# Optimization experiments

Hardware: AMD Instinct MI355X
Metric: run time of the kernel (lower is better)

Reference implementation:

```python
import jax, jax.numpy as jnp
import numpy as np

CONTEXT = 3  # config['context']
B, H, W = 8, 256, 256
NBR = 2 * CONTEXT  # number of similarity branches


def _conv(x, w, b):
    # x: [N, Cin, H, W], w: [Cout, Cin, kh, kw], SAME padding, stride 1
    y = jax.lax.conv_general_dilated(x, w, (1, 1), 'SAME',
                                     dimension_numbers=('NCHW', 'OIHW', 'NCHW'))
    return y + b[None, :, None, None]


def setup_inputs() -> dict:
    key = jax.random.key(0)
    ks = jax.random.split(key, 5)
    x = jax.random.normal(ks[0], (B, 2 * CONTEXT + 1, H, W), dtype=jnp.float32)
    # kaiming-ish scaled inits
    W1 = jax.random.normal(ks[1], (NBR, 64, 2, 3, 3), dtype=jnp.float32) * (2.0 / (64 * 9)) ** 0.5
    b1 = jnp.zeros((NBR, 64), dtype=jnp.float32)
    W2 = jax.random.normal(ks[2], (NBR, 1, 64, 1, 1), dtype=jnp.float32) * (2.0 / 1) ** 0.5 * 0.1
    b2 = jnp.zeros((NBR, 1), dtype=jnp.float32)
    Wm = jax.random.normal(ks[3], (7, 7, 3, 3), dtype=jnp.float32) * (2.0 / (7 * 9)) ** 0.5
    bm = jnp.zeros((7,), dtype=jnp.float32)
    return {'x': x, 'W1': W1, 'b1': b1, 'W2': W2, 'b2': b2, 'Wm': Wm, 'bm': bm}


def reference(x, W1, b1, W2, b2, Wm, bm):
    # mode == 'context' path just returns x; this implements the main path.
    base = x[:, CONTEXT:CONTEXT + 1]                                  # [B,1,H,W]
    checks = jnp.concatenate([x[:, :CONTEXT], x[:, CONTEXT + 1:]], axis=1)  # [B,6,H,W]
    check_e = checks[:, :, None]                                      # [B,6,1,H,W]
    base_e = jnp.broadcast_to(base[:, None], check_e.shape)           # [B,6,1,H,W]
    # channel order: pre-frames -> (base, check); post-frames -> (check, base)
    ch0 = jnp.concatenate([base_e[:, :CONTEXT], check_e[:, CONTEXT:]], axis=2 - 2 + 2)  # placeholder
    ch0 = jnp.concatenate([base_e[:, :CONTEXT], check_e[:, CONTEXT:]], axis=1)
    ch1 = jnp.concatenate([check_e[:, :CONTEXT], base_e[:, CONTEXT:]], axis=1)
    pairs = jnp.concatenate([ch0, ch1], axis=2)                       # [B,6,2,H,W]
    pairs = jnp.swapaxes(pairs, 0, 1)                                 # [6,B,2,H,W]

    def branch(pair, w1, bb1, w2, bb2):
        h = jax.nn.relu(_conv(pair, w1, bb1))                         # [B,64,H,W]
        return jax.nn.sigmoid(_conv(h, w2, bb2))                      # [B,1,H,W]

    sims = jax.vmap(branch)(pairs, W1, b1, W2, b2)                    # [6,B,1,H,W]
    weighted = sims[:, :, 0] * jnp.swapaxes(checks, 0, 1)             # [6,B,H,W]
    weighted = jnp.swapaxes(weighted, 0, 1)                           # [B,6,H,W]
    combined = jnp.concatenate([weighted[:, :CONTEXT], base, weighted[:, CONTEXT:]], axis=1)  # [B,7,H,W]
    return _conv(combined, Wm, bm)                                    # [B,7,H,W]
```

## Files before the change

### kernel.cpp

```cpp
#include <hip/hip_runtime.h>
#include <math.h>

#define Bn 8
#define Hn 256
#define Wn 256
#define HW (Hn * Wn)
#define ROWS 8
#define RP 264

typedef __attribute__((ext_vector_type(8))) short bf16x8;
typedef __attribute__((ext_vector_type(4))) float f32x4;

__device__ __forceinline__ unsigned int pk_bits(unsigned int lo,
                                                unsigned int hi) {
  return __builtin_amdgcn_perm(hi, lo, 0x07060302u);
}
__device__ __forceinline__ unsigned int pk_bf16(float lo, float hi) {
  return pk_bits(__float_as_uint(lo), __float_as_uint(hi));
}

__global__ __launch_bounds__(256) void sim_kernel(
    const float* __restrict__ x,
    const float* __restrict__ W1,
    const float* __restrict__ b1,
    const float* __restrict__ W2,
    const float* __restrict__ b2,
    float* __restrict__ comb)
{
  __shared__ float rowsF[2 * 10 * RP];
  __shared__ uint4 wq[4][64];

  int bi = blockIdx.x;
  int n  = bi >> 8;
  int b  = (bi >> 5) & 7;
  int h0 = (bi & 31) * ROWS;
  int cc = (n < 3) ? n : n + 1;
  int t = threadIdx.x;

  const float* xb     = x + (size_t)b * 7 * HW;
  const float* basep  = xb + 3 * HW;
  const float* checkp = xb + (size_t)cc * HW;

  {
    int f = t >> 6, qq = (t >> 4) & 3, m = t & 15;
    int ch = 16 * f + m;
    int bsrc = (n < 3) ? 0 : 1;
    const float* wch = W1 + ((size_t)(n * 64 + ch)) * 18;
    unsigned int kv[4];
#pragma unroll
    for (int jj = 0; jj < 4; ++jj) {
      int k0 = qq * 8 + jj * 2, k1 = k0 + 1;
      float v0 = 0.f, v1 = 0.f;
      if (k0 < 18) {
        int src = (k0 < 9) ? bsrc : 1 - bsrc;
        v0 = wch[src * 9 + (k0 < 9 ? k0 : k0 - 9)];
      }
      if (k1 < 18) {
        int src = (k1 < 9) ? bsrc : 1 - bsrc;
        v1 = wch[src * 9 + (k1 < 9 ? k1 : k1 - 9)];
      }
      kv[jj] = pk_bf16(v0, v1);
    }
    wq[f][(qq << 4) + m] = make_uint4(kv[0], kv[1], kv[2], kv[3]);
  }

  int lane = t & 63, wvid = t >> 6;
  int q = lane >> 4, m_ = lane & 15;
  float w2v[4][4], b1v[4][4];
#pragma unroll
  for (int f = 0; f < 4; ++f) {
    float4 tw = *(const float4*)&W2[n * 64 + 16 * f + 4 * q];
    float4 tb = *(const float4*)&b1[n * 64 + 16 * f + 4 * q];
    w2v[f][0] = tw.x; w2v[f][1] = tw.y; w2v[f][2] = tw.z; w2v[f][3] = tw.w;
    b1v[f][0] = tb.x; b1v[f][1] = tb.y; b1v[f][2] = tb.z; b1v[f][3] = tb.w;
  }
  float bb = b2[n];

  {
    int col = (t & 63) << 2;
#pragma unroll
    for (int it = 0; it < 5; ++it) {
      int rf = it * 4 + (t >> 6);
      int pl = (rf >= 10) ? 1 : 0;
      int j  = rf - pl * 10;
      int hh = h0 - 1 + j;
      const float* src = pl ? checkp : basep;
      float4 val = make_float4(0.f, 0.f, 0.f, 0.f);
      if ((unsigned)hh < (unsigned)Hn)
        val = *(const float4*)(src + hh * Wn + col);
      *(float4*)&rowsF[rf * RP + 4 + col] = val;
    }
    if (t < 20) {
      rowsF[t * RP + 3] = 0.f;
      rowsF[t * RP + 260] = 0.f;
    }
    if (t == 20) rowsF[0] = 0.f;
  }

  const unsigned int* rowsU = (const unsigned int*)rowsF;
  unsigned int addr[8], vbit[8];
#pragma unroll
  for (int jh = 0; jh < 8; ++jh) {
    int k = 8 * q + jh;
    if (k < 18) {
      int pl = (k >= 9) ? 1 : 0;
      int rem = k - 9 * pl;
      int rr = rem / 3, dx = rem - rr * 3;
      addr[jh] = (pl * 10 + rr) * RP + 3 + dx + wvid * 64 + m_;
      vbit[jh] = 1u;
    } else {
      addr[jh] = 0u;
      vbit[jh] = 0u;
    }
  }

  __syncthreads();

  bf16x8 afrag[4];
#pragma unroll
  for (int f = 0; f < 4; ++f) afrag[f] = *(const bf16x8*)&wq[f][lane];

  float* combcc = comb + ((size_t)b * 7 + cc) * HW;
  float* comb3  = comb + ((size_t)b * 7 + 3) * HW;
  int pxs = wvid * 64 + lane;

#pragma unroll 1
  for (int r = 0; r < ROWS; ++r) {
    int h = h0 + r;

    float g[4];
#pragma unroll
    for (int i = 0; i < 4; ++i) {
      unsigned int offs = (unsigned)(r * RP + i * 16);

      unsigned int d[8];
#pragma unroll
      for (int jh = 0; jh < 8; ++jh)
        d[jh] = rowsU[addr[jh] + vbit[jh] * offs];

      union { unsigned int u[4]; bf16x8 v; } bu;
#pragma unroll
      for (int jj = 0; jj < 4; ++jj)
        bu.u[jj] = pk_bits(d[2 * jj], d[2 * jj + 1]);
      bf16x8 bfrag = bu.v;

      f32x4 acc[4];
#pragma unroll
      for (int f = 0; f < 4; ++f) {
        acc[f][0] = b1v[f][0]; acc[f][1] = b1v[f][1];
        acc[f][2] = b1v[f][2]; acc[f][3] = b1v[f][3];
      }
#pragma unroll
      for (int f = 0; f < 4; ++f)
        acc[f] = __builtin_amdgcn_mfma_f32_16x16x32_bf16(afrag[f], bfrag,
                                                         acc[f], 0, 0, 0);

      float sp = 0.f;
#pragma unroll
      for (int f = 0; f < 4; ++f)
#pragma unroll
        for (int rr = 0; rr < 4; ++rr)
          sp = fmaf(w2v[f][rr], fmaxf(acc[f][rr], 0.f), sp);
      sp += __shfl_xor(sp, 16, 64);
      sp += __shfl_xor(sp, 32, 64);
      sp += bb;

      float e = __builtin_amdgcn_exp2f(sp * -1.442695041f);
      g[i] = __builtin_amdgcn_rcpf(1.f + e);
    }

    int hi = lane >> 4;
    float gsel = (hi == 0) ? g[0] : (hi == 1) ? g[1] : (hi == 2) ? g[2] : g[3];
    float ccv = rowsF[(10 + r + 1) * RP + 4 + pxs];
    combcc[h * Wn + pxs] = gsel * ccv;
    if (n == 0) comb3[h * Wn + pxs] = rowsF[(r + 1) * RP + 4 + pxs];
  }
}

__global__ __launch_bounds__(256) void mix_kernel(
    const float* __restrict__ comb,
    const float* __restrict__ Wm,
    const float* __restrict__ bm,
    float* __restrict__ out)
{
  __shared__ float mr[7 * 6 * RP];

  int bi = blockIdx.x;
  int b  = bi >> 6;
  int h0 = (bi & 63) << 2;
  int t = threadIdx.x;

  for (int u = t; u < 42 * 64; u += 256) {
    int rf = u >> 6;
    int col = (u & 63) << 2;
    int ic = rf / 6, j = rf - ic * 6;
    int hh = h0 - 1 + j;
    float4 v = make_float4(0.f, 0.f, 0.f, 0.f);
    if ((unsigned)hh < (unsigned)Hn)
      v = *(const float4*)(comb + ((size_t)b * 7 + ic) * HW + hh * Wn + col);
    *(float4*)&mr[rf * RP + 4 + col] = v;
  }
  if (t < 42) {
    mr[t * RP + 3] = 0.f;
    mr[t * RP + 260] = 0.f;
  }
  __syncthreads();

  int r   = t >> 6;
  int px0 = (t & 63) << 2;
  int h   = h0 + r;

  float acc[7][4];
#pragma unroll
  for (int oc = 0; oc < 7; ++oc) {
    float bv = bm[oc];
#pragma unroll
    for (int p = 0; p < 4; ++p) acc[oc][p] = bv;
  }

#pragma unroll 1
  for (int ic = 0; ic < 7; ++ic) {
    float w[3][12];
#pragma unroll
    for (int dy = 0; dy < 3; ++dy) {
      const float* rp = &mr[(ic * 6 + r + dy) * RP];
      *(float4*)&w[dy][0] = *(const float4*)(rp + px0);
      *(float4*)&w[dy][4] = *(const float4*)(rp + px0 + 4);
      *(float4*)&w[dy][8] = *(const float4*)(rp + px0 + 8);
    }
    const float* wp = Wm + ic * 9;
#pragma unroll
    for (int oc = 0; oc < 7; ++oc) {
      const float* wo = wp + oc * 63;
#pragma unroll
      for (int dy = 0; dy < 3; ++dy)
#pragma unroll
        for (int dx = 0; dx < 3; ++dx) {
          float wvv = wo[dy * 3 + dx];
#pragma unroll
          for (int p = 0; p < 4; ++p)
            acc[oc][p] = fmaf(wvv, w[dy][3 + p + dx], acc[oc][p]);
        }
    }
  }

  float* ob = out + (size_t)b * 7 * HW + h * Wn + px0;
#pragma unroll
  for (int oc = 0; oc < 7; ++oc)
    *(float4*)(ob + (size_t)oc * HW) =
        make_float4(acc[oc][0], acc[oc][1], acc[oc][2], acc[oc][3]);
}

extern "C" void kernel_launch(void* const* d_in, const int* in_sizes, int n_in,
                              void* d_out, int out_size, void* d_ws, size_t ws_size,
                              hipStream_t stream) {
  const float* x  = (const float*)d_in[0];
  const float* W1 = (const float*)d_in[1];
  const float* b1 = (const float*)d_in[2];
  const float* W2 = (const float*)d_in[3];
  const float* b2 = (const float*)d_in[4];
  const float* Wm = (const float*)d_in[5];
  const float* bm = (const float*)d_in[6];
  float* out  = (float*)d_out;
  float* comb = (float*)d_ws;

  sim_kernel<<<6 * 8 * (Hn / ROWS), 256, 0, stream>>>(x, W1, b1, W2, b2, comb);
  mix_kernel<<<8 * (Hn / 4), 256, 0, stream>>>(comb, Wm, bm, out);
}
```

Measured before the change: 121.6 us.

## Reorder MFMA K taps, batch LDS loads, pass bias as accumulator, shrink mix tiles

In the similarity kernel the 18 conv taps are permuted across the K lanes through constant lookup tables. Padding lanes now read a dedicated zero strip instead of address 0. LDS reads for two 16-pixel groups are issued together per half, and the b1 vector is passed directly as the MFMA accumulator input, which cuts register copies. The mix kernel switches from 4 rows by 4 pixels to 2 rows by 2 pixels per thread and doubles the block count, trading extra halo reloads (4 rows loaded per 2 output rows) for more parallelism and fewer registers per thread.

```diff
diff --git a/kernel.cpp b/kernel.cpp
--- a/kernel.cpp
+++ b/kernel.cpp
@@ -7,6 +7,7 @@
 #define HW (Hn * Wn)
 #define ROWS 8
 #define RP 264
+#define ZW (20 * RP)
 
 typedef __attribute__((ext_vector_type(8))) short bf16x8;
 typedef __attribute__((ext_vector_type(4))) float f32x4;
@@ -18,6 +19,10 @@
 __device__ __forceinline__ unsigned int pk_bf16(float lo, float hi) {
   return pk_bits(__float_as_uint(lo), __float_as_uint(hi));
 }
+
+__device__ __constant__ const int T0c[8] = {0, 1, 2, 9, 10, 11, 3, 4};
+__device__ __constant__ const int T1c[8] = {6, 7, 8, 15, 16, 17, 12, 13};
+__device__ __constant__ const int T2c[8] = {5, 14, -1, -1, -1, -1, -1, -1};
 
 __global__ __launch_bounds__(256) void sim_kernel(
     const float* __restrict__ x,
@@ -27,7 +32,7 @@
     const float* __restrict__ b2,
     float* __restrict__ comb)
 {
-  __shared__ float rowsF[2 * 10 * RP];
+  __shared__ float rowsF[20 * RP + 64];
   __shared__ uint4 wq[4][64];
 
   int bi = blockIdx.x;
@@ -43,36 +48,41 @@
 
   {
     int f = t >> 6, qq = (t >> 4) & 3, m = t & 15;
-    int ch = 16 * f + m;
     int bsrc = (n < 3) ? 0 : 1;
-    const float* wch = W1 + ((size_t)(n * 64 + ch)) * 18;
+    const float* wch = W1 + ((size_t)(n * 64 + 16 * f + m)) * 18;
     unsigned int kv[4];
 #pragma unroll
     for (int jj = 0; jj < 4; ++jj) {
-      int k0 = qq * 8 + jj * 2, k1 = k0 + 1;
-      float v0 = 0.f, v1 = 0.f;
-      if (k0 < 18) {
-        int src = (k0 < 9) ? bsrc : 1 - bsrc;
-        v0 = wch[src * 9 + (k0 < 9 ? k0 : k0 - 9)];
-      }
-      if (k1 < 18) {
-        int src = (k1 < 9) ? bsrc : 1 - bsrc;
-        v1 = wch[src * 9 + (k1 < 9 ? k1 : k1 - 9)];
-      }
-      kv[jj] = pk_bf16(v0, v1);
+      int ja = 2 * jj, jb = 2 * jj + 1;
+      int ta = (qq == 0) ? T0c[ja] : (qq == 1) ? T1c[ja]
+               : (qq == 2) ? T2c[ja] : -1;
+      int tb = (qq == 0) ? T0c[jb] : (qq == 1) ? T1c[jb]
+               : (qq == 2) ? T2c[jb] : -1;
+      float va = 0.f, vb = 0.f;
+      if (ta >= 0) {
+        int pl = ta / 9, rem = ta - pl * 9;
+        va = wch[(pl ? 1 - bsrc : bsrc) * 9 + rem];
+      }
+      if (tb >= 0) {
+        int pl = tb / 9, rem = tb - pl * 9;
+        vb = wch[(pl ? 1 - bsrc : bsrc) * 9 + rem];
+      }
+      kv[jj] = pk_bf16(va, vb);
     }
     wq[f][(qq << 4) + m] = make_uint4(kv[0], kv[1], kv[2], kv[3]);
   }
 
   int lane = t & 63, wvid = t >> 6;
   int q = lane >> 4, m_ = lane & 15;
-  float w2v[4][4], b1v[4][4];
+  float w2v[4][4];
+  f32x4 b1vv[4];
 #pragma unroll
   for (int f = 0; f < 4; ++f) {
     float4 tw = *(const float4*)&W2[n * 64 + 16 * f + 4 * q];
     float4 tb = *(const float4*)&b1[n * 64 + 16 * f + 4 * q];
     w2v[f][0] = tw.x; w2v[f][1] = tw.y; w2v[f][2] = tw.z; w2v[f][3] = tw.w;
-    b1v[f][0] = tb.x; b1v[f][1] = tb.y; b1v[f][2] = tb.z; b1v[f][3] = tb.w;
+    b1vv[f][0] = tb.x; b1vv[f][1] = tb.y;
+    b1vv[f][2] = tb.z; b1vv[f][3] = tb.w;
   }
   float bb = b2[n];
 
@@ -94,22 +104,22 @@
       rowsF[t * RP + 3] = 0.f;
       rowsF[t * RP + 260] = 0.f;
     }
-    if (t == 20) rowsF[0] = 0.f;
+    if (t >= 192) rowsF[ZW + (t - 192)] = 0.f;
   }
 
   const unsigned int* rowsU = (const unsigned int*)rowsF;
   unsigned int addr[8], vbit[8];
 #pragma unroll
   for (int jh = 0; jh < 8; ++jh) {
-    int k = 8 * q + jh;
-    if (k < 18) {
-      int pl = (k >= 9) ? 1 : 0;
-      int rem = k - 9 * pl;
+    int tap = (q == 0) ? T0c[jh] : (q == 1) ? T1c[jh]
+              : (q == 2) ? T2c[jh] : -1;
+    if (tap >= 0) {
+      int pl = tap / 9, rem = tap - pl * 9;
       int rr = rem / 3, dx = rem - rr * 3;
       addr[jh] = (pl * 10 + rr) * RP + 3 + dx + wvid * 64 + m_;
       vbit[jh] = 1u;
     } else {
-      addr[jh] = 0u;
+      addr[jh] = (unsigned)ZW;
       vbit[jh] = 0u;
     }
   }
@@ -127,46 +137,48 @@
 #pragma unroll 1
   for (int r = 0; r < ROWS; ++r) {
     int h = h0 + r;
+    unsigned int rowoff = (unsigned)(r * RP);
+
+    unsigned int base[8];
+#pragma unroll
+    for (int jh = 0; jh < 8; ++jh) base[jh] = addr[jh] + vbit[jh] * rowoff;
 
     float g[4];
 #pragma unroll
-    for (int i = 0; i < 4; ++i) {
-      unsigned int offs = (unsigned)(r * RP + i * 16);
-
-      unsigned int d[8];
-#pragma unroll
-      for (int jh = 0; jh < 8; ++jh)
-        d[jh] = rowsU[addr[jh] + vbit[jh] * offs];
-
-      union { unsigned int u[4]; bf16x8 v; } bu;
-#pragma unroll
-      for (int jj = 0; jj < 4; ++jj)
-        bu.u[jj] = pk_bits(d[2 * jj], d[2 * jj + 1]);
-      bf16x8 bfrag = bu.v;
-
-      f32x4 acc[4];
-#pragma unroll
-      for (int f = 0; f < 4; ++f) {
-        acc[f][0] = b1v[f][0]; acc[f][1] = b1v[f][1];
-        acc[f][2] = b1v[f][2]; acc[f][3] = b1v[f][3];
-      }
-#pragma unroll
-      for (int f = 0; f < 4; ++f)
-        acc[f] = __builtin_amdgcn_mfma_f32_16x16x32_bf16(afrag[f], bfrag,
-                                                         acc[f], 0, 0, 0);
-
-      float sp = 0.f;
-#pragma unroll
-      for (int f = 0; f < 4; ++f)
-#pragma unroll
-        for (int rr = 0; rr < 4; ++rr)
-          sp = fmaf(w2v[f][rr], fmaxf(acc[f][rr], 0.f), sp);
-      sp += __shfl_xor(sp, 16, 64);
-      sp += __shfl_xor(sp, 32, 64);
-      sp += bb;
-
-      float e = __builtin_amdgcn_exp2f(sp * -1.442695041f);
-      g[i] = __builtin_amdgcn_rcpf(1.f + e);
+    for (int half = 0; half < 2; ++half) {
+      unsigned int dlo[8], dhi[8];
+#pragma unroll
+      for (int jh = 0; jh < 8; ++jh) {
+        dlo[jh] = rowsU[base[jh] + half * 32];
+        dhi[jh] = rowsU[base[jh] + half * 32 + 16];
+      }
+#pragma unroll
+      for (int j = 0; j < 2; ++j) {
+        const unsigned int* d = j ? dhi : dlo;
+        union { unsigned int u[4]; bf16x8 v; } bu;
+#pragma unroll
+        for (int jj = 0; jj < 4; ++jj)
+          bu.u[jj] = pk_bits(d[2 * jj], d[2 * jj + 1]);
+
+        f32x4 acc[4];
+#pragma unroll
+        for (int f = 0; f < 4; ++f)
+          acc[f] = __builtin_amdgcn_mfma_f32_16x16x32_bf16(afrag[f], bu.v,
+                                                           b1vv[f], 0, 0, 0);
+
+        float sp = 0.f;
+#pragma unroll
+        for (int f = 0; f < 4; ++f)
+#pragma unroll
+          for (int rr = 0; rr < 4; ++rr)
+            sp = fmaf(w2v[f][rr], fmaxf(acc[f][rr], 0.f), sp);
+        sp += __shfl_xor(sp, 16, 64);
+        sp += __shfl_xor(sp, 32, 64);
+        sp += bb;
+
+        float e = __builtin_amdgcn_exp2f(sp * -1.442695041f);
+        g[2 * half + j] = __builtin_amdgcn_rcpf(1.f + e);
+      }
     }
 
     int hi = lane >> 4;
@@ -183,50 +195,49 @@
     const float* __restrict__ bm,
     float* __restrict__ out)
 {
-  __shared__ float mr[7 * 6 * RP];
+  __shared__ float mr[28 * RP];
 
   int bi = blockIdx.x;
-  int b  = bi >> 6;
-  int h0 = (bi & 63) << 2;
+  int b  = bi >> 7;
+  int h0 = (bi & 127) << 1;
   int t = threadIdx.x;
 
-  for (int u = t; u < 42 * 64; u += 256) {
+  for (int u = t; u < 28 * 64; u += 256) {
     int rf = u >> 6;
     int col = (u & 63) << 2;
-    int ic = rf / 6, j = rf - ic * 6;
+    int ic = rf >> 2, j = rf & 3;
     int hh = h0 - 1 + j;
     float4 v = make_float4(0.f, 0.f, 0.f, 0.f);
     if ((unsigned)hh < (unsigned)Hn)
       v = *(const float4*)(comb + ((size_t)b * 7 + ic) * HW + hh * Wn + col);
     *(float4*)&mr[rf * RP + 4 + col] = v;
   }
-  if (t < 42) {
+  if (t < 28) {
     mr[t * RP + 3] = 0.f;
     mr[t * RP + 260] = 0.f;
   }
   __syncthreads();
 
-  int r   = t >> 6;
-  int px0 = (t & 63) << 2;
+  int r   = t >> 7;
+  int px0 = (t & 127) << 1;
   int h   = h0 + r;
 
-  float acc[7][4];
+  float acc[7][2];
 #pragma unroll
   for (int oc = 0; oc < 7; ++oc) {
     float bv = bm[oc];
-#pragma unroll
-    for (int p = 0; p < 4; ++p) acc[oc][p] = bv;
+    acc[oc][0] = bv;
+    acc[oc][1] = bv;
   }
 
 #pragma unroll 1
   for (int ic = 0; ic < 7; ++ic) {
-    float w[3][12];
+    float w[3][4];
 #pragma unroll
     for (int dy = 0; dy < 3; ++dy) {
-      const float* rp = &mr[(ic * 6 + r + dy) * RP];
-      *(float4*)&w[dy][0] = *(const float4*)(rp + px0);
-      *(float4*)&w[dy][4] = *(const float4*)(rp + px0 + 4);
-      *(float4*)&w[dy][8] = *(const float4*)(rp + px0 + 8);
+      const float* rp = &mr[(ic * 4 + r + dy) * RP + 3 + px0];
+      w[dy][0] = rp[0]; w[dy][1] = rp[1];
+      w[dy][2] = rp[2]; w[dy][3] = rp[3];
     }
     const float* wp = Wm + ic * 9;
 #pragma unroll
@@ -237,9 +248,8 @@
 #pragma unroll
         for (int dx = 0; dx < 3; ++dx) {
           float wvv = wo[dy * 3 + dx];
-#pragma unroll
-          for (int p = 0; p < 4; ++p)
-            acc[oc][p] = fmaf(wvv, w[dy][3 + p + dx], acc[oc][p]);
+          acc[oc][0] = fmaf(wvv, w[dy][0 + dx], acc[oc][0]);
+          acc[oc][1] = fmaf(wvv, w[dy][1 + dx], acc[oc][1]);
         }
     }
   }
@@ -247,8 +257,7 @@
   float* ob = out + (size_t)b * 7 * HW + h * Wn + px0;
 #pragma unroll
   for (int oc = 0; oc < 7; ++oc)
-    *(float4*)(ob + (size_t)oc * HW) =
-        make_float4(acc[oc][0], acc[oc][1], acc[oc][2], acc[oc][3]);
+    *(float2*)(ob + (size_t)oc * HW) = make_float2(acc[oc][0], acc[oc][1]);
 }
 
 extern "C" void kernel_launch(void* const* d_in, const int* in_sizes, int n_in,
@@ -265,5 +274,5 @@
   float* comb = (float*)d_ws;
 
   sim_kernel<<<6 * 8 * (Hn / ROWS), 256, 0, stream>>>(x, W1, b1, W2, b2, comb);
-  mix_kernel<<<8 * (Hn / 4), 256, 0, stream>>>(comb, Wm, bm, out);
-}
+  mix_kernel<<<8 * (Hn / 2), 256, 0, stream>>>(comb, Wm, bm, out);
+}
```

Measured after the change: 119.9 us. No clear change (-1.4%).
